# Optimization experiments

Hardware: AMD Instinct MI355X
Metric: run time of the kernel (lower is better)

## Reference

```python
import jax, jax.numpy as jnp
import numpy as np

N, F, B, H = 4096, 64, 16, 8  # nodes, feat dim, graphs, GAT heads


def _graph():
    # symmetric random graph (avg deg ~8), plus exact 2-hop and 3-hop edge lists
    # (this reproduces torch_sparse.spspmm with coalesced=True on the boolean structure)
    rng = np.random.default_rng(0)
    s = rng.integers(0, N, 8192)
    d = rng.integers(0, N, 8192)
    m = s != d
    s, d = s[m], d[m]
    rows = np.concatenate([s, d]).astype(np.int64)
    cols = np.concatenate([d, s]).astype(np.int64)
    key = np.unique(rows * N + cols)
    rows, cols = key // N, key % N
    A = np.zeros((N, N), np.float32)
    A[rows, cols] = 1.0
    A2 = (A @ A) > 0
    A3 = (A2.astype(np.float32) @ A) > 0
    np.fill_diagonal(A2, False)  # GATConv/GCNConv remove then re-add self-loops
    np.fill_diagonal(A3, False)
    e1 = np.stack([rows, cols]).astype(np.int64)
    e2 = np.stack(np.nonzero(A2)).astype(np.int64)
    e3 = np.stack(np.nonzero(A3)).astype(np.int64)
    return e1, e2, e3


def _sl(ei, n):
    loops = jnp.arange(n, dtype=ei.dtype)
    return jnp.concatenate([ei, jnp.stack([loops, loops])], axis=1)


def _seg_softmax(logits, seg, n):
    m = jax.ops.segment_max(logits, seg, num_segments=n)
    e = jnp.exp(logits - m[seg])
    s = jax.ops.segment_sum(e, seg, num_segments=n)
    return e / s[seg]


def _gat(x, ei, W, a_src, a_dst, b, heads):
    # PyG GATConv: per-head linear, edge attention logits, softmax over incoming edges
    n = x.shape[0]
    d = a_src.shape[1]
    h = (x @ W).reshape(n, heads, d)  # [N,H,D]
    src, dst = ei[0], ei[1]
    al = jnp.einsum('nhd,hd->nh', h, a_src)
    ar = jnp.einsum('nhd,hd->nh', h, a_dst)
    logit = jax.nn.leaky_relu(al[src] + ar[dst], 0.2)  # [E,H]
    alpha = _seg_softmax(logit, dst, n)
    out = jax.ops.segment_sum(alpha[:, :, None] * h[src], dst, num_segments=n)
    return out.reshape(n, heads * d) + b


def _gcn(x, ei, W, b):
    n = x.shape[0]
    src, dst = ei[0], ei[1]
    h = x @ W
    deg = jax.ops.segment_sum(jnp.ones(src.shape, x.dtype), dst, num_segments=n)
    dinv = jnp.where(deg > 0, deg ** -0.5, 0.0)
    norm = dinv[src] * dinv[dst]
    return jax.ops.segment_sum(norm[:, None] * h[src], dst, num_segments=n) + b


def setup_inputs():
    key = jax.random.key(0)
    ks = iter(jax.random.split(key, 40))
    e1, e2, e3 = _graph()
    p = lambda *shape: jax.random.normal(next(ks), shape, jnp.float32) * 0.1
    return dict(
        x=jax.random.normal(next(ks), (N, F), jnp.float32),
        edge_index=jnp.asarray(e1), edge_index2=jnp.asarray(e2), edge_index3=jnp.asarray(e3),
        batch=jnp.asarray(np.repeat(np.arange(B), N // B)),
        g1_W=p(F, H * F), g1_as=p(H, F), g1_ad=p(H, F), g1_b=p(H * F),
        g2_W=p(H * F, F), g2_as=p(1, F), g2_ad=p(1, F), g2_b=p(F),
        gfc_W=p(F, F), gfc_b=p(F), gfc1_W=p(F, 128), gfc1_b=p(128),
        gout_W=p(128, F), gout_b=p(F),
        c2_W=p(F, 2 * F), c2_b=p(2 * F), c3_W=p(2 * F, 4 * F), c3_b=p(4 * F),
        A_W=p(4 * F, F), A_b=p(F), B_W=p(2 * F, F), B_b=p(F),
        Wih=p(F, 3 * F), Whh=p(F, 3 * F), bih=p(3 * F), bhh=p(3 * F),
        f1_W=p(F, 128), f1_b=p(128), f2_W=p(128, 120), f2_b=p(120),
    )


def reference(x, edge_index, edge_index2, edge_index3, batch,
              g1_W, g1_as, g1_ad, g1_b, g2_W, g2_as, g2_ad, g2_b,
              gfc_W, gfc_b, gfc1_W, gfc1_b, gout_W, gout_b,
              c2_W, c2_b, c3_W, c3_b, A_W, A_b, B_W, B_b,
              Wih, Whh, bih, bhh, f1_W, f1_b, f2_W, f2_b):
    n = x.shape[0]
    e1, e2, e3 = _sl(edge_index, n), _sl(edge_index2, n), _sl(edge_index3, n)

    def gat_block(xin, ei):  # inner GAT module (eval mode: dropouts are identity)
        h = jax.nn.elu(_gat(xin, ei, g1_W, g1_as, g1_ad, g1_b, H))
        h = jax.nn.relu(_gat(h, ei, g2_W, g2_as, g2_ad, g2_b, 1))
        h = jax.nn.relu(h @ gfc_W + gfc_b)
        h = jax.nn.relu(h @ gfc1_W + gfc1_b)
        return h @ gout_W + gout_b

    h1 = jax.nn.relu(gat_block(x, e1))
    h2 = jax.nn.relu(_gcn(h1, e1, c2_W, c2_b))
    h3 = jax.nn.relu(_gcn(h2, e1, c3_W, c3_b))            # [N,4F]
    h4 = jax.nn.relu(gat_block(x, e2))
    h5 = jax.nn.relu(_gcn(h4, e2, c2_W, c2_b))            # [N,2F]
    h6 = jax.nn.relu(gat_block(x, e3))                     # [N,F]

    # GateUpdate
    b_ = h5 @ B_W + B_b
    a_ = h3 @ A_W + A_b
    z = jax.nn.sigmoid(a_ + b_)
    hg = z * b_ + (1 - z) * a_
    # GRUCell(h6, hg)
    gi = h6 @ Wih + bih
    gh = hg @ Whh + bhh
    r = jax.nn.sigmoid(gi[:, :F] + gh[:, :F])
    zz = jax.nn.sigmoid(gi[:, F:2 * F] + gh[:, F:2 * F])
    nn_ = jnp.tanh(gi[:, 2 * F:] + r * gh[:, 2 * F:])
    cc = (1 - zz) * nn_ + zz * hg

    g = jax.ops.segment_max(cc, batch, num_segments=B)    # global_max_pool -> [B,F]
    g = jax.nn.relu(g @ f1_W + f1_b)
    return g @ f2_W + f2_b                                 # [B,120]
```

## Files before the change

kernel.cpp:

```cpp
#include <hip/hip_runtime.h>
#include <math.h>

#define NN 4096
#define NG 16
#define WB() __builtin_amdgcn_wave_barrier()

__global__ void rowptr3_kernel(const int* __restrict__ ea, int Ea,
                               const int* __restrict__ eb, int Eb,
                               const int* __restrict__ ec, int Ec,
                               int* __restrict__ rpa, int* __restrict__ rpb, int* __restrict__ rpc){
    int t = blockIdx.x * blockDim.x + threadIdx.x;
    int set = t / (NN + 1), i = t % (NN + 1);
    if (set >= 3) return;
    const int* e0 = set == 0 ? ea : set == 1 ? eb : ec;
    int E        = set == 0 ? Ea : set == 1 ? Eb : Ec;
    int* rp      = set == 0 ? rpa : set == 1 ? rpb : rpc;
    if (i == NN){ rp[NN] = E; return; }
    int lo = 0, hi = E;
    while (lo < hi){ int mid = (lo + hi) >> 1; if (e0[mid] < i) lo = mid + 1; else hi = mid; }
    rp[i] = lo;
}

__global__ void dinv2_kernel(const int* __restrict__ rp1, const int* __restrict__ rp2,
                             float* __restrict__ dinv1, float* __restrict__ dinv2){
    int t = blockIdx.x * blockDim.x + threadIdx.x;
    int set = t >> 12, i = t & (NN - 1);
    if (set >= 2) return;
    const int* rp = set ? rp2 : rp1;
    float deg = (float)(rp[i+1] - rp[i] + 1);
    (set ? dinv2 : dinv1)[i] = 1.0f / sqrtf(deg);
}

__global__ __launch_bounds__(256)
void gemm_kernel(const float* __restrict__ A, const float* __restrict__ W,
                 const float* __restrict__ bias, float* __restrict__ C,
                 int K, int Nc, int act){
    __shared__ float As[64][17];
    __shared__ float Bs[16][64];
    const int tid = threadIdx.x;
    const int tx = tid & 15, ty = tid >> 4;
    const int row0 = blockIdx.y * 64, col0 = blockIdx.x * 64;
    float acc[4][4] = {};
    for (int k0 = 0; k0 < K; k0 += 16){
        {   int idx = tid * 4; int r = idx >> 4, kk = idx & 15;
            float4 av = *reinterpret_cast<const float4*>(&A[(size_t)(row0 + r) * K + k0 + kk]);
            As[r][kk+0]=av.x; As[r][kk+1]=av.y; As[r][kk+2]=av.z; As[r][kk+3]=av.w; }
        {   int idx = tid * 4; int r = idx >> 6, cc = idx & 63;
            float4 wv = *reinterpret_cast<const float4*>(&W[(size_t)(k0 + r) * Nc + col0 + cc]);
            *reinterpret_cast<float4*>(&Bs[r][cc]) = wv; }
        __syncthreads();
        #pragma unroll
        for (int kk = 0; kk < 16; ++kk){
            float a[4], b[4];
            #pragma unroll
            for (int i = 0; i < 4; ++i) a[i] = As[ty*4+i][kk];
            #pragma unroll
            for (int j = 0; j < 4; ++j) b[j] = Bs[kk][tx*4+j];
            #pragma unroll
            for (int i = 0; i < 4; ++i)
                #pragma unroll
                for (int j = 0; j < 4; ++j) acc[i][j] += a[i]*b[j];
        }
        __syncthreads();
    }
    #pragma unroll
    for (int i = 0; i < 4; ++i){
        int r = row0 + ty*4 + i;
        #pragma unroll
        for (int j = 0; j < 4; ++j){
            int c = col0 + tx*4 + j;
            float v = acc[i][j] + (bias ? bias[c] : 0.0f);
            if (act == 1) v = fmaxf(v, 0.0f);
            C[(size_t)r * Nc + c] = v;
        }
    }
}

__global__ __launch_bounds__(256)
void gemm_attn8_kernel(const float* __restrict__ A, const float* __restrict__ W,
                       float* __restrict__ C,
                       const float* __restrict__ a_src, const float* __restrict__ a_dst,
                       float* __restrict__ al, float* __restrict__ ar){
    __shared__ float As[64][17];
    __shared__ float Bs[16][64];
    __shared__ float redal[64][17];
    __shared__ float redar[64][17];
    const int tid = threadIdx.x;
    const int tx = tid & 15, ty = tid >> 4;
    const int row0 = blockIdx.y * 64, col0 = blockIdx.x * 64;
    const int K = 64, Nc = 512;
    float acc[4][4] = {};
    for (int k0 = 0; k0 < K; k0 += 16){
        {   int idx = tid * 4; int r = idx >> 4, kk = idx & 15;
            float4 av = *reinterpret_cast<const float4*>(&A[(size_t)(row0 + r) * K + k0 + kk]);
            As[r][kk+0]=av.x; As[r][kk+1]=av.y; As[r][kk+2]=av.z; As[r][kk+3]=av.w; }
        {   int idx = tid * 4; int r = idx >> 6, cc = idx & 63;
            float4 wv = *reinterpret_cast<const float4*>(&W[(size_t)(k0 + r) * Nc + col0 + cc]);
            *reinterpret_cast<float4*>(&Bs[r][cc]) = wv; }
        __syncthreads();
        #pragma unroll
        for (int kk = 0; kk < 16; ++kk){
            float a[4], b[4];
            #pragma unroll
            for (int i = 0; i < 4; ++i) a[i] = As[ty*4+i][kk];
            #pragma unroll
            for (int j = 0; j < 4; ++j) b[j] = Bs[kk][tx*4+j];
            #pragma unroll
            for (int i = 0; i < 4; ++i)
                #pragma unroll
                for (int j = 0; j < 4; ++j) acc[i][j] += a[i]*b[j];
        }
        __syncthreads();
    }
    float pal[4] = {0.f,0.f,0.f,0.f}, par[4] = {0.f,0.f,0.f,0.f};
    #pragma unroll
    for (int j = 0; j < 4; ++j){
        int c = col0 + tx*4 + j;
        float as = a_src[c], ad = a_dst[c];
        #pragma unroll
        for (int i = 0; i < 4; ++i){
            pal[i] += acc[i][j] * as;
            par[i] += acc[i][j] * ad;
        }
    }
    #pragma unroll
    for (int i = 0; i < 4; ++i){
        int r = row0 + ty*4 + i;
        #pragma unroll
        for (int j = 0; j < 4; ++j)
            C[(size_t)r * Nc + col0 + tx*4 + j] = acc[i][j];
        redal[ty*4+i][tx] = pal[i];
        redar[ty*4+i][tx] = par[i];
    }
    __syncthreads();
    if (tid < 64){
        float sa = 0.f, sr = 0.f;
        #pragma unroll
        for (int t = 0; t < 16; ++t){ sa += redal[tid][t]; sr += redar[tid][t]; }
        al[(size_t)(row0 + tid)*8 + blockIdx.x] = sa;
        ar[(size_t)(row0 + tid)*8 + blockIdx.x] = sr;
    }
}

__global__ __launch_bounds__(256)
void gemm32_kernel(const float* __restrict__ A, const float* __restrict__ W,
                   const float* __restrict__ bias, float* __restrict__ C,
                   int K, int Nc, int act){
    __shared__ float As[32][17];
    __shared__ float Bs[16][64];
    const int tid = threadIdx.x;
    const int tx = tid & 15, ty = tid >> 4;
    const int row0 = blockIdx.y * 32, col0 = blockIdx.x * 64;
    float acc[2][4] = {};
    for (int k0 = 0; k0 < K; k0 += 16){
        {   int idx = tid * 2; int r = idx >> 4, kk = idx & 15;
            float2 av = *reinterpret_cast<const float2*>(&A[(size_t)(row0 + r) * K + k0 + kk]);
            As[r][kk] = av.x; As[r][kk+1] = av.y; }
        {   int idx = tid * 4; int r = idx >> 6, cc = idx & 63;
            *reinterpret_cast<float4*>(&Bs[r][cc]) =
                *reinterpret_cast<const float4*>(&W[(size_t)(k0 + r) * Nc + col0 + cc]); }
        __syncthreads();
        #pragma unroll
        for (int kk = 0; kk < 16; ++kk){
            float a0 = As[ty*2][kk], a1 = As[ty*2+1][kk];
            float b[4];
            #pragma unroll
            for (int j = 0; j < 4; ++j) b[j] = Bs[kk][tx*4+j];
            #pragma unroll
            for (int j = 0; j < 4; ++j){ acc[0][j] += a0*b[j]; acc[1][j] += a1*b[j]; }
        }
        __syncthreads();
    }
    #pragma unroll
    for (int i = 0; i < 2; ++i){
        int r = row0 + ty*2 + i;
        #pragma unroll
        for (int j = 0; j < 4; ++j){
            int c = col0 + tx*4 + j;
            float v = acc[i][j] + (bias ? bias[c] : 0.0f);
            if (act == 1) v = fmaxf(v, 0.0f);
            C[(size_t)r * Nc + c] = v;
        }
    }
}

__global__ __launch_bounds__(256)
void gemm32_attn1_kernel(const float* __restrict__ A, const float* __restrict__ W,
                         float* __restrict__ C,
                         const float* __restrict__ a_src, const float* __restrict__ a_dst,
                         float* __restrict__ al, float* __restrict__ ar){
    __shared__ float As[32][17];
    __shared__ float Bs[16][64];
    __shared__ float redal[32][17];
    __shared__ float redar[32][17];
    const int tid = threadIdx.x;
    const int tx = tid & 15, ty = tid >> 4;
    const int row0 = blockIdx.y * 32;
    const int K = 512, Nc = 64;
    float acc[2][4] = {};
    for (int k0 = 0; k0 < K; k0 += 16){
        {   int idx = tid * 2; int r = idx >> 4, kk = idx & 15;
            float2 av = *reinterpret_cast<const float2*>(&A[(size_t)(row0 + r) * K + k0 + kk]);
            As[r][kk] = av.x; As[r][kk+1] = av.y; }
        {   int idx = tid * 4; int r = idx >> 6, cc = idx & 63;
            *reinterpret_cast<float4*>(&Bs[r][cc]) =
                *reinterpret_cast<const float4*>(&W[(size_t)(k0 + r) * Nc + cc]); }
        __syncthreads();
        #pragma unroll
        for (int kk = 0; kk < 16; ++kk){
            float a0 = As[ty*2][kk], a1 = As[ty*2+1][kk];
            float b[4];
            #pragma unroll
            for (int j = 0; j < 4; ++j) b[j] = Bs[kk][tx*4+j];
            #pragma unroll
            for (int j = 0; j < 4; ++j){ acc[0][j] += a0*b[j]; acc[1][j] += a1*b[j]; }
        }
        __syncthreads();
    }
    float pal[2] = {0.f,0.f}, par[2] = {0.f,0.f};
    #pragma unroll
    for (int j = 0; j < 4; ++j){
        int c = tx*4 + j;
        float as = a_src[c], ad = a_dst[c];
        pal[0] += acc[0][j]*as; pal[1] += acc[1][j]*as;
        par[0] += acc[0][j]*ad; par[1] += acc[1][j]*ad;
    }
    #pragma unroll
    for (int i = 0; i < 2; ++i){
        int r = row0 + ty*2 + i;
        #pragma unroll
        for (int j = 0; j < 4; ++j)
            C[(size_t)r * Nc + tx*4 + j] = acc[i][j];
        redal[ty*2+i][tx] = pal[i];
        redar[ty*2+i][tx] = par[i];
    }
    __syncthreads();
    if (tid < 32){
        float sa = 0.f, sr = 0.f;
        #pragma unroll
        for (int t = 0; t < 16; ++t){ sa += redal[tid][t]; sr += redar[tid][t]; }
        al[row0 + tid] = sa;
        ar[row0 + tid] = sr;
    }
}

__global__ __launch_bounds__(64)
void gat_agg8_p2_kernel(const float* __restrict__ hfeat,
                        const float* __restrict__ al, const float* __restrict__ ar,
                        const int* __restrict__ rpA, const int* __restrict__ rpB, const int* __restrict__ rpC,
                        const int* __restrict__ clA, const int* __restrict__ clB, const int* __restrict__ clC,
                        const float* __restrict__ bias, float* __restrict__ out){
    const int bid = blockIdx.x;
    const int g = bid >> 1, half = bid & 1;
    const int set = g >> 12, i = g & (NN - 1);
    const int lane = threadIdx.x;
    const int* rowptr = set == 0 ? rpA : set == 1 ? rpB : rpC;
    const int* cols   = set == 0 ? clA : set == 1 ? clB : clC;
    const int start = rowptr[i], end = rowptr[i+1];
    const int deg = end - start;
    const int hb = half * 4;
    const int c0 = half * 256 + 4 * lane;
    const int hr = lane >> 4;

    float4 arv = *reinterpret_cast<const float4*>(&ar[(size_t)i*8 + hb]);
    float ar_i[4] = {arv.x, arv.y, arv.z, arv.w};
    float4 alv = *reinterpret_cast<const float4*>(&al[(size_t)i*8 + hb]);
    float al_i[4] = {alv.x, alv.y, alv.z, alv.w};

    float mh[4], sh[4];
    #pragma unroll
    for (int h = 0; h < 4; ++h){ mh[h] = -1e30f; sh[h] = 0.f; }
    for (int k = start + lane; k < end; k += 64){
        int j = cols[k];
        float4 av = *reinterpret_cast<const float4*>(&al[(size_t)j*8 + hb]);
        float a4[4] = {av.x, av.y, av.z, av.w};
        #pragma unroll
        for (int h = 0; h < 4; ++h){
            float x = a4[h] + ar_i[h];
            x = x >= 0.f ? x : 0.2f * x;
            float mn = fmaxf(mh[h], x);
            sh[h] = sh[h] * __expf(mh[h] - mn) + __expf(x - mn);
            mh[h] = mn;
        }
    }
    if (lane == 0){
        #pragma unroll
        for (int h = 0; h < 4; ++h){
            float x = al_i[h] + ar_i[h];
            x = x >= 0.f ? x : 0.2f * x;
            float mn = fmaxf(mh[h], x);
            sh[h] = sh[h] * __expf(mh[h] - mn) + __expf(x - mn);
            mh[h] = mn;
        }
    }
    #pragma unroll
    for (int off = 1; off < 64; off <<= 1){
        #pragma unroll
        for (int h = 0; h < 4; ++h){
            float m2 = __shfl_xor(mh[h], off), s2 = __shfl_xor(sh[h], off);
            float mn = fmaxf(mh[h], m2);
            sh[h] = sh[h] * __expf(mh[h] - mn) + s2 * __expf(m2 - mn);
            mh[h] = mn;
        }
    }

    __shared__ int   sbuf[64];
    __shared__ float wbuf[64][5];
    float4 A0 = {0.f, 0.f, 0.f, 0.f};
    for (int k0 = 0; k0 < deg; k0 += 64){
        int cnt = min(64, deg - k0);
        if (lane < cnt){
            int j = cols[start + k0 + lane];
            sbuf[lane] = j;
            float4 av = *reinterpret_cast<const float4*>(&al[(size_t)j*8 + hb]);
            float a4[4] = {av.x, av.y, av.z, av.w};
            #pragma unroll
            for (int h = 0; h < 4; ++h){
                float x = a4[h] + ar_i[h];
                x = x >= 0.f ? x : 0.2f * x;
                wbuf[lane][h] = __expf(x - mh[h]);
            }
        }
        __syncthreads();
        int e = 0;
        for (; e + 8 <= cnt; e += 8){
            int j0 = sbuf[e],   j1 = sbuf[e+1], j2 = sbuf[e+2], j3 = sbuf[e+3];
            int j4 = sbuf[e+4], j5 = sbuf[e+5], j6 = sbuf[e+6], j7 = sbuf[e+7];
            float4 v0 = *reinterpret_cast<const float4*>(&hfeat[(size_t)j0*512 + c0]);
            float4 v1 = *reinterpret_cast<const float4*>(&hfeat[(size_t)j1*512 + c0]);
            float4 v2 = *reinterpret_cast<const float4*>(&hfeat[(size_t)j2*512 + c0]);
            float4 v3 = *reinterpret_cast<const float4*>(&hfeat[(size_t)j3*512 + c0]);
            float4 v4 = *reinterpret_cast<const float4*>(&hfeat[(size_t)j4*512 + c0]);
            float4 v5 = *reinterpret_cast<const float4*>(&hfeat[(size_t)j5*512 + c0]);
            float4 v6 = *reinterpret_cast<const float4*>(&hfeat[(size_t)j6*512 + c0]);
            float4 v7 = *reinterpret_cast<const float4*>(&hfeat[(size_t)j7*512 + c0]);
            float w0 = wbuf[e  ][hr], w1 = wbuf[e+1][hr], w2 = wbuf[e+2][hr], w3 = wbuf[e+3][hr];
            float w4 = wbuf[e+4][hr], w5 = wbuf[e+5][hr], w6 = wbuf[e+6][hr], w7 = wbuf[e+7][hr];
            A0.x += w0*v0.x; A0.y += w0*v0.y; A0.z += w0*v0.z; A0.w += w0*v0.w;
            A0.x += w1*v1.x; A0.y += w1*v1.y; A0.z += w1*v1.z; A0.w += w1*v1.w;
            A0.x += w2*v2.x; A0.y += w2*v2.y; A0.z += w2*v2.z; A0.w += w2*v2.w;
            A0.x += w3*v3.x; A0.y += w3*v3.y; A0.z += w3*v3.z; A0.w += w3*v3.w;
            A0.x += w4*v4.x; A0.y += w4*v4.y; A0.z += w4*v4.z; A0.w += w4*v4.w;
            A0.x += w5*v5.x; A0.y += w5*v5.y; A0.z += w5*v5.z; A0.w += w5*v5.w;
            A0.x += w6*v6.x; A0.y += w6*v6.y; A0.z += w6*v6.z; A0.w += w6*v6.w;
            A0.x += w7*v7.x; A0.y += w7*v7.y; A0.z += w7*v7.z; A0.w += w7*v7.w;
        }
        for (; e < cnt; ++e){
            int j = sbuf[e];
            float4 v = *reinterpret_cast<const float4*>(&hfeat[(size_t)j*512 + c0]);
            float w = wbuf[e][hr];
            A0.x += w*v.x; A0.y += w*v.y; A0.z += w*v.z; A0.w += w*v.w;
        }
        __syncthreads();
    }
    float x = al_i[hr] + ar_i[hr];
    x = x >= 0.f ? x : 0.2f * x;
    float ws = __expf(x - mh[hr]);
    float4 hv = *reinterpret_cast<const float4*>(&hfeat[(size_t)i*512 + c0]);
    A0.x += ws*hv.x; A0.y += ws*hv.y; A0.z += ws*hv.z; A0.w += ws*hv.w;
    float inv = 1.f / sh[hr];
    float4 bv = *reinterpret_cast<const float4*>(&bias[c0]);
    float4 o;
    o.x = A0.x*inv + bv.x; o.y = A0.y*inv + bv.y;
    o.z = A0.z*inv + bv.z; o.w = A0.w*inv + bv.w;
    o.x = o.x > 0.f ? o.x : __expf(o.x) - 1.f;
    o.y = o.y > 0.f ? o.y : __expf(o.y) - 1.f;
    o.z = o.z > 0.f ? o.z : __expf(o.z) - 1.f;
    o.w = o.w > 0.f ? o.w : __expf(o.w) - 1.f;
    *reinterpret_cast<float4*>(&out[(size_t)g*512 + c0]) = o;
}

template<int BLOCK, int NHEADS>
__global__ __launch_bounds__(BLOCK)
void gat_agg_kernel(const float* __restrict__ hfeat,
                    const float* __restrict__ al, const float* __restrict__ ar,
                    const int* __restrict__ rpA, const int* __restrict__ rpB, const int* __restrict__ rpC,
                    const int* __restrict__ clA, const int* __restrict__ clB, const int* __restrict__ clC,
                    const float* __restrict__ bias, float* __restrict__ out,
                    int act, int sharedfeat){
    constexpr int TD    = NHEADS * 64;
    constexpr int CHUNK = BLOCK / NHEADS;
    const int bid = blockIdx.x;
    const int set = bid >> 12, i = bid & (NN - 1);
    const int tid = threadIdx.x;
    const int* rowptr = set == 0 ? rpA : set == 1 ? rpB : rpC;
    const int* cols   = set == 0 ? clA : set == 1 ? clB : clC;
    const int base = sharedfeat ? 0 : set * NN;
    const int start = rowptr[i], end = rowptr[i+1];

    float al_i[NHEADS], ar_i[NHEADS];
    #pragma unroll
    for (int h = 0; h < NHEADS; ++h){
        al_i[h] = al[(size_t)(base + i)*NHEADS + h];
        ar_i[h] = ar[(size_t)(base + i)*NHEADS + h];
    }
    float m[NHEADS], s[NHEADS];
    #pragma unroll
    for (int h = 0; h < NHEADS; ++h){ m[h] = -1e30f; s[h] = 0.f; }
    for (int k = start + tid; k < end; k += BLOCK){
        int j = cols[k];
        #pragma unroll
        for (int h = 0; h < NHEADS; ++h){
            float x = al[(size_t)(base + j)*NHEADS + h] + ar_i[h];
            x = x >= 0.f ? x : 0.2f * x;
            float mn = fmaxf(m[h], x);
            s[h] = s[h] * __expf(m[h] - mn) + __expf(x - mn);
            m[h] = mn;
        }
    }
    if (tid == 0){
        #pragma unroll
        for (int h = 0; h < NHEADS; ++h){
            float x = al_i[h] + ar_i[h];
            x = x >= 0.f ? x : 0.2f * x;
            float mn = fmaxf(m[h], x);
            s[h] = s[h] * __expf(m[h] - mn) + __expf(x - mn);
            m[h] = mn;
        }
    }
    #pragma unroll
    for (int off = 1; off < 64; off <<= 1){
        #pragma unroll
        for (int h = 0; h < NHEADS; ++h){
            float m2 = __shfl_xor(m[h], off), s2 = __shfl_xor(s[h], off);
            float mn = fmaxf(m[h], m2);
            s[h] = s[h] * __expf(m[h] - mn) + s2 * __expf(m2 - mn);
            m[h] = mn;
        }
    }

    __shared__ int   sbuf[CHUNK];
    __shared__ float wbuf[CHUNK][NHEADS];
    const int deg = end - start;
    float p0 = 0.f, p1 = 0.f, p2 = 0.f, p3 = 0.f;
    for (int k0 = 0; k0 < deg; k0 += CHUNK){
        int cnt = min(CHUNK, deg - k0);
        if (tid < cnt) sbuf[tid] = cols[start + k0 + tid];
        __syncthreads();
        if (tid < cnt){
            float x = al[(size_t)(base + sbuf[tid])*NHEADS] + ar_i[0];
            x = x >= 0.f ? x : 0.2f * x;
            wbuf[tid][0] = __expf(x - m[0]);
        }
        __syncthreads();
        int e = 0;
        for (; e + 8 <= cnt; e += 8){
            int j0 = sbuf[e],   j1 = sbuf[e+1], j2 = sbuf[e+2], j3 = sbuf[e+3];
            int j4 = sbuf[e+4], j5 = sbuf[e+5], j6 = sbuf[e+6], j7 = sbuf[e+7];
            float v0 = hfeat[(size_t)(base + j0)*TD + tid];
            float v1 = hfeat[(size_t)(base + j1)*TD + tid];
            float v2 = hfeat[(size_t)(base + j2)*TD + tid];
            float v3 = hfeat[(size_t)(base + j3)*TD + tid];
            float v4 = hfeat[(size_t)(base + j4)*TD + tid];
            float v5 = hfeat[(size_t)(base + j5)*TD + tid];
            float v6 = hfeat[(size_t)(base + j6)*TD + tid];
            float v7 = hfeat[(size_t)(base + j7)*TD + tid];
            p0 += wbuf[e  ][0] * v0; p1 += wbuf[e+1][0] * v1;
            p2 += wbuf[e+2][0] * v2; p3 += wbuf[e+3][0] * v3;
            p0 += wbuf[e+4][0] * v4; p1 += wbuf[e+5][0] * v5;
            p2 += wbuf[e+6][0] * v6; p3 += wbuf[e+7][0] * v7;
        }
        for (; e < cnt; ++e)
            p0 += wbuf[e][0] * hfeat[(size_t)(base + sbuf[e])*TD + tid];
        __syncthreads();
    }
    float acc = (p0 + p1) + (p2 + p3);
    float x = al_i[0] + ar_i[0];
    x = x >= 0.f ? x : 0.2f * x;
    acc += __expf(x - m[0]) * hfeat[(size_t)(base + i)*TD + tid];
    float v = acc / s[0] + bias[tid];
    if (act == 1) v = fmaxf(v, 0.f);
    else          v = v > 0.f ? v : __expf(v) - 1.f;
    out[(size_t)bid*TD + tid] = v;
}

template<int DIM>
__global__ __launch_bounds__(DIM)
void gcn_agg_kernel(const float* __restrict__ h,
                    const int* __restrict__ rpA, const int* __restrict__ rpB,
                    const int* __restrict__ clA, const int* __restrict__ clB,
                    const float* __restrict__ dvA, const float* __restrict__ dvB,
                    const float* __restrict__ bias, float* __restrict__ out){
    const int bid = blockIdx.x;
    const int set = bid >> 12, i = bid & (NN - 1);
    const int* rowptr = set ? rpB : rpA;
    const int* cols   = set ? clB : clA;
    const float* dinv = set ? dvB : dvA;
    const int c = threadIdx.x;
    const int start = rowptr[i], end = rowptr[i+1];
    const float di = dinv[i];
    const size_t rbase = (size_t)(set * NN) * DIM;
    float self = di * di * h[(size_t)bid * DIM + c];
    float p0 = 0.f, p1 = 0.f, p2 = 0.f, p3 = 0.f;
    int k = start;
    for (; k + 8 <= end; k += 8){
        int j0 = cols[k],   j1 = cols[k+1], j2 = cols[k+2], j3 = cols[k+3];
        int j4 = cols[k+4], j5 = cols[k+5], j6 = cols[k+6], j7 = cols[k+7];
        float v0 = h[rbase + (size_t)j0 * DIM + c];
        float v1 = h[rbase + (size_t)j1 * DIM + c];
        float v2 = h[rbase + (size_t)j2 * DIM + c];
        float v3 = h[rbase + (size_t)j3 * DIM + c];
        float v4 = h[rbase + (size_t)j4 * DIM + c];
        float v5 = h[rbase + (size_t)j5 * DIM + c];
        float v6 = h[rbase + (size_t)j6 * DIM + c];
        float v7 = h[rbase + (size_t)j7 * DIM + c];
        p0 += dinv[j0] * v0; p1 += dinv[j1] * v1;
        p2 += dinv[j2] * v2; p3 += dinv[j3] * v3;
        p0 += dinv[j4] * v4; p1 += dinv[j5] * v5;
        p2 += dinv[j6] * v6; p3 += dinv[j7] * v7;
    }
    for (; k < end; ++k){
        int j = cols[k];
        p0 += dinv[j] * h[rbase + (size_t)j * DIM + c];
    }
    float acc = self + di * ((p0 + p1) + (p2 + p3));
    out[(size_t)bid * DIM + c] = fmaxf(acc + bias[c], 0.f);
}

__global__ __launch_bounds__(256)
void gate_gru_kernel(const float* __restrict__ h3, const float* __restrict__ h5,
                     const float* __restrict__ h6,
                     const float* __restrict__ A_W, const float* __restrict__ A_b,
                     const float* __restrict__ B_W, const float* __restrict__ B_b,
                     const float* __restrict__ Wih, const float* __restrict__ bih,
                     const float* __restrict__ Whh, const float* __restrict__ bhh,
                     float* __restrict__ cc){
    __shared__ float l3[4][256];
    __shared__ float l5[4][128];
    __shared__ float l6[4][64];
    __shared__ float lhg[4][64];
    const int lane = threadIdx.x & 63, wid = threadIdx.x >> 6;
    const int r = blockIdx.x * 4 + wid;
    for (int c = lane; c < 256; c += 64) l3[wid][c] = h3[(size_t)r*256 + c];
    for (int c = lane; c < 128; c += 64) l5[wid][c] = h5[(size_t)r*128 + c];
    l6[wid][lane] = h6[(size_t)r*64 + lane];
    WB();
    float a = A_b[lane];
    #pragma unroll 8
    for (int k = 0; k < 256; ++k) a += l3[wid][k] * A_W[k*64 + lane];
    float b = B_b[lane];
    #pragma unroll 8
    for (int k = 0; k < 128; ++k) b += l5[wid][k] * B_W[k*64 + lane];
    float z = 1.f / (1.f + expf(-(a + b)));
    float hg = z * b + (1.f - z) * a;
    lhg[wid][lane] = hg;
    WB();
    float gi0 = bih[lane], gi1 = bih[64 + lane], gi2 = bih[128 + lane];
    float gh0 = bhh[lane], gh1 = bhh[64 + lane], gh2 = bhh[128 + lane];
    #pragma unroll 4
    for (int k = 0; k < 64; ++k){
        float v6 = l6[wid][k], vh = lhg[wid][k];
        gi0 += v6 * Wih[k*192 + lane];
        gi1 += v6 * Wih[k*192 + 64 + lane];
        gi2 += v6 * Wih[k*192 + 128 + lane];
        gh0 += vh * Whh[k*192 + lane];
        gh1 += vh * Whh[k*192 + 64 + lane];
        gh2 += vh * Whh[k*192 + 128 + lane];
    }
    float rr = 1.f / (1.f + expf(-(gi0 + gh0)));
    float zz = 1.f / (1.f + expf(-(gi1 + gh1)));
    float nn = tanhf(gi2 + rr * gh2);
    cc[(size_t)r*64 + lane] = (1.f - zz) * nn + zz * hg;
}

__global__ __launch_bounds__(256)
void head_kernel(const float* __restrict__ cc,
                 const float* __restrict__ f1_W, const float* __restrict__ f1_b,
                 const float* __restrict__ f2_W, const float* __restrict__ f2_b,
                 float* __restrict__ out){
    const int b = blockIdx.x, tid = threadIdx.x;
    const int c = tid & 63, grp = tid >> 6;
    __shared__ float red4[4][64];
    __shared__ float gmax[64];
    __shared__ float fgs[128];
    const float* base = cc + (size_t)(b * (NN / NG)) * 64;
    float m = -1e30f;
    #pragma unroll 8
    for (int n = grp; n < NN / NG; n += 4) m = fmaxf(m, base[n * 64 + c]);
    red4[grp][c] = m;
    __syncthreads();
    if (tid < 64)
        gmax[tid] = fmaxf(fmaxf(red4[0][tid], red4[1][tid]),
                          fmaxf(red4[2][tid], red4[3][tid]));
    __syncthreads();
    if (tid < 128){
        float acc = 0.f;
        #pragma unroll
        for (int k = 0; k < 64; ++k) acc += gmax[k] * f1_W[k * 128 + tid];
        fgs[tid] = fmaxf(acc + f1_b[tid], 0.f);
    }
    __syncthreads();
    if (tid < 120){
        float acc = 0.f;
        #pragma unroll
        for (int k = 0; k < 128; ++k) acc += fgs[k] * f2_W[k * 120 + tid];
        out[b * 120 + tid] = acc + f2_b[tid];
    }
}

extern "C" void kernel_launch(void* const* d_in, const int* in_sizes, int n_in,
                              void* d_out, int out_size, void* d_ws, size_t ws_size,
                              hipStream_t stream){
    const float* x  = (const float*)d_in[0];
    const int* e1 = (const int*)d_in[1]; const int E1 = in_sizes[1] / 2;
    const int* e2 = (const int*)d_in[2]; const int E2 = in_sizes[2] / 2;
    const int* e3 = (const int*)d_in[3]; const int E3 = in_sizes[3] / 2;
    const float* g1_W  = (const float*)d_in[5];
    const float* g1_as = (const float*)d_in[6];
    const float* g1_ad = (const float*)d_in[7];
    const float* g1_b  = (const float*)d_in[8];
    const float* g2_W  = (const float*)d_in[9];
    const float* g2_as = (const float*)d_in[10];
    const float* g2_ad = (const float*)d_in[11];
    const float* g2_b  = (const float*)d_in[12];
    const float* gfc_W = (const float*)d_in[13];
    const float* gfc_b = (const float*)d_in[14];
    const float* gfc1_W= (const float*)d_in[15];
    const float* gfc1_b= (const float*)d_in[16];
    const float* gout_W= (const float*)d_in[17];
    const float* gout_b= (const float*)d_in[18];
    const float* c2_W  = (const float*)d_in[19];
    const float* c2_b  = (const float*)d_in[20];
    const float* c3_W  = (const float*)d_in[21];
    const float* c3_b  = (const float*)d_in[22];
    const float* A_W   = (const float*)d_in[23];
    const float* A_b   = (const float*)d_in[24];
    const float* B_W   = (const float*)d_in[25];
    const float* B_b   = (const float*)d_in[26];
    const float* Wih   = (const float*)d_in[27];
    const float* Whh   = (const float*)d_in[28];
    const float* bih   = (const float*)d_in[29];
    const float* bhh   = (const float*)d_in[30];
    const float* f1_W  = (const float*)d_in[31];
    const float* f1_b  = (const float*)d_in[32];
    const float* f2_W  = (const float*)d_in[33];
    const float* f2_b  = (const float*)d_in[34];
    float* out = (float*)d_out;

    int* ip = (int*)d_ws;
    int* rp1 = ip; int* rp2 = ip + 4100; int* rp3 = ip + 8200;
    float* fb = (float*)(ip + 12300);
    size_t o = 0;
    auto alloc = [&](size_t nf){ float* p = fb + o; o += nf; return p; };
    float* dinv1 = alloc(NN);
    float* dinv2 = alloc(NN);
    float* hbuf  = alloc((size_t)NN*512);
    float* al1   = alloc((size_t)NN*8);
    float* ar1   = alloc((size_t)NN*8);
    float* bigA  = alloc((size_t)3*NN*512);
    float* t2    = alloc((size_t)3*NN*64);
    float* al2   = alloc((size_t)3*NN);
    float* ar2   = alloc((size_t)3*NN);
    (void)ws_size; (void)n_in; (void)out_size;

    float* eluo3 = bigA;
    float* g2o   = bigA;
    float* fc1   = bigA + (size_t)786432;
    float* fc2   = bigA + (size_t)1572864;
    float* houts = hbuf;
    float* h1    = houts;
    float* h6    = houts + (size_t)2*NN*64;
    float* gcnx2 = bigA + (size_t)3145728;
    float* h25   = bigA + (size_t)4194304;
    float* h2    = h25;
    float* h5    = h25 + (size_t)NN*128;
    float* gcnx3 = bigA;
    float* h3    = bigA + (size_t)1048576;
    float* ccb   = bigA + (size_t)4456448;
    const int* cols1 = e1 + E1; const int* cols2 = e2 + E2; const int* cols3 = e3 + E3;

    rowptr3_kernel<<<(3*(NN+1)+255)/256, 256, 0, stream>>>(e1, E1, e2, E2, e3, E3, rp1, rp2, rp3);
    dinv2_kernel<<<2*NN/256, 256, 0, stream>>>(rp1, rp2, dinv1, dinv2);

    gemm_attn8_kernel<<<dim3(8, 64), 256, 0, stream>>>(x, g1_W, hbuf, g1_as, g1_ad, al1, ar1);
    gat_agg8_p2_kernel<<<6*NN, 64, 0, stream>>>(hbuf, al1, ar1,
        rp1, rp2, rp3, cols1, cols2, cols3, g1_b, eluo3);
    gemm32_attn1_kernel<<<dim3(1, 384), 256, 0, stream>>>(eluo3, g2_W, t2, g2_as, g2_ad, al2, ar2);
    gat_agg_kernel<64,1><<<3*NN, 64, 0, stream>>>(t2, al2, ar2,
        rp1, rp2, rp3, cols1, cols2, cols3, g2_b, g2o, 1, 0);
    gemm32_kernel<<<dim3(1, 384), 256, 0, stream>>>(g2o, gfc_W, gfc_b, fc1, 64, 64, 1);
    gemm_kernel<<<dim3(2, 192), 256, 0, stream>>>(fc1, gfc1_W, gfc1_b, fc2, 64, 128, 1);
    gemm32_kernel<<<dim3(1, 384), 256, 0, stream>>>(fc2, gout_W, gout_b, houts, 128, 64, 1);

    gemm_kernel<<<dim3(2, 128), 256, 0, stream>>>(houts, c2_W, nullptr, gcnx2, 64, 128, 0);
    gcn_agg_kernel<128><<<2*NN, 128, 0, stream>>>(gcnx2, rp1, rp2, cols1, cols2,
                                                  dinv1, dinv2, c2_b, h25);
    gemm_kernel<<<dim3(4, 64), 256, 0, stream>>>(h2, c3_W, nullptr, gcnx3, 128, 256, 0);
    gcn_agg_kernel<256><<<NN, 256, 0, stream>>>(gcnx3, rp1, rp1, cols1, cols1,
                                                dinv1, dinv1, c3_b, h3);

    gate_gru_kernel<<<NN/4, 256, 0, stream>>>(h3, h5, h6, A_W, A_b, B_W, B_b,
                                              Wih, bih, Whh, bhh, ccb);

    head_kernel<<<NG, 256, 0, stream>>>(ccb, f1_W, f1_b, f2_W, f2_b, out);
}
```

Before: 352.1 us.

## Replace per-node online softmax max pass with global max-based upper bound

A small reduction kernel now computes the global maximum of the source attention logit per head. Because leaky_relu is monotone, leaky_relu(max_al + ar_i) upper-bounds every incoming edge logit, so each node can use it as the softmax shift. This removes the separate pass over neighbours that computed an online max and sum, and the sum is now accumulated inside the main aggregation loop. The second-layer GAT aggregation is rewritten the same way as a dedicated one-head kernel. The cost is two extra single-block launches, plus a risk of exp underflow if a node's logits sit far below the global bound.

```diff
diff --git a/kernel.cpp b/kernel.cpp
--- a/kernel.cpp
+++ b/kernel.cpp
@@ -29,6 +29,31 @@
     const int* rp = set ? rp2 : rp1;
     float deg = (float)(rp[i+1] - rp[i] + 1);
     (set ? dinv2 : dinv1)[i] = 1.0f / sqrtf(deg);
+}
+
+template<int NH>
+__global__ __launch_bounds__(256)
+void max_al_kernel(const float* __restrict__ al, int n, float* __restrict__ M){
+    __shared__ float red[4 * NH];
+    float mx[NH];
+    #pragma unroll
+    for (int h = 0; h < NH; ++h) mx[h] = -1e30f;
+    for (int r = threadIdx.x; r < n; r += 256)
+        #pragma unroll
+        for (int h = 0; h < NH; ++h) mx[h] = fmaxf(mx[h], al[(size_t)r*NH + h]);
+    #pragma unroll
+    for (int h = 0; h < NH; ++h){
+        float v = mx[h];
+        #pragma unroll
+        for (int off = 1; off < 64; off <<= 1) v = fmaxf(v, __shfl_xor(v, off));
+        if ((threadIdx.x & 63) == 0) red[(threadIdx.x >> 6) * NH + h] = v;
+    }
+    __syncthreads();
+    if (threadIdx.x < NH){
+        float m = fmaxf(fmaxf(red[0*NH + threadIdx.x], red[1*NH + threadIdx.x]),
+                        fmaxf(red[2*NH + threadIdx.x], red[3*NH + threadIdx.x]));
+        M[threadIdx.x] = m;
+    }
 }
 
 __global__ __launch_bounds__(256)
@@ -247,6 +272,7 @@
 __global__ __launch_bounds__(64)
 void gat_agg8_p2_kernel(const float* __restrict__ hfeat,
                         const float* __restrict__ al, const float* __restrict__ ar,
+                        const float* __restrict__ M8,
                         const int* __restrict__ rpA, const int* __restrict__ rpB, const int* __restrict__ rpC,
                         const int* __restrict__ clA, const int* __restrict__ clB, const int* __restrict__ clC,
                         const float* __restrict__ bias, float* __restrict__ out){
@@ -266,47 +292,19 @@
     float ar_i[4] = {arv.x, arv.y, arv.z, arv.w};
     float4 alv = *reinterpret_cast<const float4*>(&al[(size_t)i*8 + hb]);
     float al_i[4] = {alv.x, alv.y, alv.z, alv.w};
-
-    float mh[4], sh[4];
-    #pragma unroll
-    for (int h = 0; h < 4; ++h){ mh[h] = -1e30f; sh[h] = 0.f; }
-    for (int k = start + lane; k < end; k += 64){
-        int j = cols[k];
-        float4 av = *reinterpret_cast<const float4*>(&al[(size_t)j*8 + hb]);
-        float a4[4] = {av.x, av.y, av.z, av.w};
-        #pragma unroll
-        for (int h = 0; h < 4; ++h){
-            float x = a4[h] + ar_i[h];
-            x = x >= 0.f ? x : 0.2f * x;
-            float mn = fmaxf(mh[h], x);
-            sh[h] = sh[h] * __expf(mh[h] - mn) + __expf(x - mn);
-            mh[h] = mn;
-        }
-    }
-    if (lane == 0){
-        #pragma unroll
-        for (int h = 0; h < 4; ++h){
-            float x = al_i[h] + ar_i[h];
-            x = x >= 0.f ? x : 0.2f * x;
-            float mn = fmaxf(mh[h], x);
-            sh[h] = sh[h] * __expf(mh[h] - mn) + __expf(x - mn);
-            mh[h] = mn;
-        }
-    }
-    #pragma unroll
-    for (int off = 1; off < 64; off <<= 1){
-        #pragma unroll
-        for (int h = 0; h < 4; ++h){
-            float m2 = __shfl_xor(mh[h], off), s2 = __shfl_xor(sh[h], off);
-            float mn = fmaxf(mh[h], m2);
-            sh[h] = sh[h] * __expf(mh[h] - mn) + s2 * __expf(m2 - mn);
-            mh[h] = mn;
-        }
+    float4 Mv = *reinterpret_cast<const float4*>(&M8[hb]);
+    float Ma[4] = {Mv.x, Mv.y, Mv.z, Mv.w};
+    float mh[4];
+    #pragma unroll
+    for (int h = 0; h < 4; ++h){
+        float t = Ma[h] + ar_i[h];
+        mh[h] = t >= 0.f ? t : 0.2f * t;
     }
 
     __shared__ int   sbuf[64];
     __shared__ float wbuf[64][5];
     float4 A0 = {0.f, 0.f, 0.f, 0.f};
+    float sacc[4] = {0.f, 0.f, 0.f, 0.f};
     for (int k0 = 0; k0 < deg; k0 += 64){
         int cnt = min(64, deg - k0);
         if (lane < cnt){
@@ -318,7 +316,9 @@
             for (int h = 0; h < 4; ++h){
                 float x = a4[h] + ar_i[h];
                 x = x >= 0.f ? x : 0.2f * x;
-                wbuf[lane][h] = __expf(x - mh[h]);
+                float w = __expf(x - mh[h]);
+                wbuf[lane][h] = w;
+                sacc[h] += w;
             }
         }
         __syncthreads();
@@ -353,12 +353,17 @@
         }
         __syncthreads();
     }
+    #pragma unroll
+    for (int off = 1; off < 64; off <<= 1){
+        #pragma unroll
+        for (int h = 0; h < 4; ++h) sacc[h] += __shfl_xor(sacc[h], off);
+    }
     float x = al_i[hr] + ar_i[hr];
     x = x >= 0.f ? x : 0.2f * x;
     float ws = __expf(x - mh[hr]);
     float4 hv = *reinterpret_cast<const float4*>(&hfeat[(size_t)i*512 + c0]);
     A0.x += ws*hv.x; A0.y += ws*hv.y; A0.z += ws*hv.z; A0.w += ws*hv.w;
-    float inv = 1.f / sh[hr];
+    float inv = 1.f / (sacc[hr] + ws);
     float4 bv = *reinterpret_cast<const float4*>(&bias[c0]);
     float4 o;
     o.x = A0.x*inv + bv.x; o.y = A0.y*inv + bv.y;
@@ -370,108 +375,73 @@
     *reinterpret_cast<float4*>(&out[(size_t)g*512 + c0]) = o;
 }
 
-template<int BLOCK, int NHEADS>
-__global__ __launch_bounds__(BLOCK)
-void gat_agg_kernel(const float* __restrict__ hfeat,
-                    const float* __restrict__ al, const float* __restrict__ ar,
-                    const int* __restrict__ rpA, const int* __restrict__ rpB, const int* __restrict__ rpC,
-                    const int* __restrict__ clA, const int* __restrict__ clB, const int* __restrict__ clC,
-                    const float* __restrict__ bias, float* __restrict__ out,
-                    int act, int sharedfeat){
-    constexpr int TD    = NHEADS * 64;
-    constexpr int CHUNK = BLOCK / NHEADS;
+__global__ __launch_bounds__(64)
+void gat_agg1_kernel(const float* __restrict__ hfeat,
+                     const float* __restrict__ al, const float* __restrict__ ar,
+                     const float* __restrict__ M1,
+                     const int* __restrict__ rpA, const int* __restrict__ rpB, const int* __restrict__ rpC,
+                     const int* __restrict__ clA, const int* __restrict__ clB, const int* __restrict__ clC,
+                     const float* __restrict__ bias, float* __restrict__ out){
     const int bid = blockIdx.x;
     const int set = bid >> 12, i = bid & (NN - 1);
     const int tid = threadIdx.x;
     const int* rowptr = set == 0 ? rpA : set == 1 ? rpB : rpC;
     const int* cols   = set == 0 ? clA : set == 1 ? clB : clC;
-    const int base = sharedfeat ? 0 : set * NN;
+    const int base = set * NN;
     const int start = rowptr[i], end = rowptr[i+1];
-
-    float al_i[NHEADS], ar_i[NHEADS];
-    #pragma unroll
-    for (int h = 0; h < NHEADS; ++h){
-        al_i[h] = al[(size_t)(base + i)*NHEADS + h];
-        ar_i[h] = ar[(size_t)(base + i)*NHEADS + h];
-    }
-    float m[NHEADS], s[NHEADS];
-    #pragma unroll
-    for (int h = 0; h < NHEADS; ++h){ m[h] = -1e30f; s[h] = 0.f; }
-    for (int k = start + tid; k < end; k += BLOCK){
-        int j = cols[k];
-        #pragma unroll
-        for (int h = 0; h < NHEADS; ++h){
-            float x = al[(size_t)(base + j)*NHEADS + h] + ar_i[h];
+    const int deg = end - start;
+
+    const float al_i = al[(size_t)base + i];
+    const float ar_i = ar[(size_t)base + i];
+    float mt = M1[0] + ar_i;
+    const float m = mt >= 0.f ? mt : 0.2f * mt;
+
+    __shared__ int   sbuf[64];
+    __shared__ float wbv[64];
+    float p0 = 0.f, p1 = 0.f, p2 = 0.f, p3 = 0.f;
+    float sacc = 0.f;
+    for (int k0 = 0; k0 < deg; k0 += 64){
+        int cnt = min(64, deg - k0);
+        if (tid < cnt){
+            int j = cols[start + k0 + tid];
+            sbuf[tid] = j;
+            float x = al[(size_t)base + j] + ar_i;
             x = x >= 0.f ? x : 0.2f * x;
-            float mn = fmaxf(m[h], x);
-            s[h] = s[h] * __expf(m[h] - mn) + __expf(x - mn);
-            m[h] = mn;
-        }
-    }
-    if (tid == 0){
-        #pragma unroll
-        for (int h = 0; h < NHEADS; ++h){
-            float x = al_i[h] + ar_i[h];
-            x = x >= 0.f ? x : 0.2f * x;
-            float mn = fmaxf(m[h], x);
-            s[h] = s[h] * __expf(m[h] - mn) + __expf(x - mn);
-            m[h] = mn;
-        }
-    }
-    #pragma unroll
-    for (int off = 1; off < 64; off <<= 1){
-        #pragma unroll
-        for (int h = 0; h < NHEADS; ++h){
-            float m2 = __shfl_xor(m[h], off), s2 = __shfl_xor(s[h], off);
-            float mn = fmaxf(m[h], m2);
-            s[h] = s[h] * __expf(m[h] - mn) + s2 * __expf(m2 - mn);
-            m[h] = mn;
-        }
-    }
-
-    __shared__ int   sbuf[CHUNK];
-    __shared__ float wbuf[CHUNK][NHEADS];
-    const int deg = end - start;
-    float p0 = 0.f, p1 = 0.f, p2 = 0.f, p3 = 0.f;
-    for (int k0 = 0; k0 < deg; k0 += CHUNK){
-        int cnt = min(CHUNK, deg - k0);
-        if (tid < cnt) sbuf[tid] = cols[start + k0 + tid];
-        __syncthreads();
-        if (tid < cnt){
-            float x = al[(size_t)(base + sbuf[tid])*NHEADS] + ar_i[0];
-            x = x >= 0.f ? x : 0.2f * x;
-            wbuf[tid][0] = __expf(x - m[0]);
+            float w = __expf(x - m);
+            wbv[tid] = w;
+            sacc += w;
         }
         __syncthreads();
         int e = 0;
         for (; e + 8 <= cnt; e += 8){
             int j0 = sbuf[e],   j1 = sbuf[e+1], j2 = sbuf[e+2], j3 = sbuf[e+3];
             int j4 = sbuf[e+4], j5 = sbuf[e+5], j6 = sbuf[e+6], j7 = sbuf[e+7];
-            float v0 = hfeat[(size_t)(base + j0)*TD + tid];
-            float v1 = hfeat[(size_t)(base + j1)*TD + tid];
-            float v2 = hfeat[(size_t)(base + j2)*TD + tid];
-            float v3 = hfeat[(size_t)(base + j3)*TD + tid];
-            float v4 = hfeat[(size_t)(base + j4)*TD + tid];
-            float v5 = hfeat[(size_t)(base + j5)*TD + tid];
-            float v6 = hfeat[(size_t)(base + j6)*TD + tid];
-            float v7 = hfeat[(size_t)(base + j7)*TD + tid];
-            p0 += wbuf[e  ][0] * v0; p1 += wbuf[e+1][0] * v1;
-            p2 += wbuf[e+2][0] * v2; p3 += wbuf[e+3][0] * v3;
-            p0 += wbuf[e+4][0] * v4; p1 += wbuf[e+5][0] * v5;
-            p2 += wbuf[e+6][0] * v6; p3 += wbuf[e+7][0] * v7;
+            float v0 = hfeat[(size_t)(base + j0)*64 + tid];
+            float v1 = hfeat[(size_t)(base + j1)*64 + tid];
+            float v2 = hfeat[(size_t)(base + j2)*64 + tid];
+            float v3 = hfeat[(size_t)(base + j3)*64 + tid];
+            float v4 = hfeat[(size_t)(base + j4)*64 + tid];
+            float v5 = hfeat[(size_t)(base + j5)*64 + tid];
+            float v6 = hfeat[(size_t)(base + j6)*64 + tid];
+            float v7 = hfeat[(size_t)(base + j7)*64 + tid];
+            p0 += wbv[e  ] * v0; p1 += wbv[e+1] * v1;
+            p2 += wbv[e+2] * v2; p3 += wbv[e+3] * v3;
+            p0 += wbv[e+4] * v4; p1 += wbv[e+5] * v5;
+            p2 += wbv[e+6] * v6; p3 += wbv[e+7] * v7;
         }
         for (; e < cnt; ++e)
-            p0 += wbuf[e][0] * hfeat[(size_t)(base + sbuf[e])*TD + tid];
-        __syncthreads();
-    }
+            p0 += wbv[e] * hfeat[(size_t)(base + sbuf[e])*64 + tid];
+        __syncthreads();
+    }
+    #pragma unroll
+    for (int off = 1; off < 64; off <<= 1) sacc += __shfl_xor(sacc, off);
     float acc = (p0 + p1) + (p2 + p3);
-    float x = al_i[0] + ar_i[0];
+    float x = al_i + ar_i;
     x = x >= 0.f ? x : 0.2f * x;
-    acc += __expf(x - m[0]) * hfeat[(size_t)(base + i)*TD + tid];
-    float v = acc / s[0] + bias[tid];
-    if (act == 1) v = fmaxf(v, 0.f);
-    else          v = v > 0.f ? v : __expf(v) - 1.f;
-    out[(size_t)bid*TD + tid] = v;
+    float ws = __expf(x - m);
+    acc += ws * hfeat[(size_t)(base + i)*64 + tid];
+    float v = acc / (sacc + ws) + bias[tid];
+    out[(size_t)bid*64 + tid] = fmaxf(v, 0.f);
 }
 
 template<int DIM>
@@ -644,6 +614,8 @@
     auto alloc = [&](size_t nf){ float* p = fb + o; o += nf; return p; };
     float* dinv1 = alloc(NN);
     float* dinv2 = alloc(NN);
+    float* M8buf = alloc(8);
+    float* M1buf = alloc(8);
     float* hbuf  = alloc((size_t)NN*512);
     float* al1   = alloc((size_t)NN*8);
     float* ar1   = alloc((size_t)NN*8);
@@ -673,11 +645,13 @@
     dinv2_kernel<<<2*NN/256, 256, 0, stream>>>(rp1, rp2, dinv1, dinv2);
 
     gemm_attn8_kernel<<<dim3(8, 64), 256, 0, stream>>>(x, g1_W, hbuf, g1_as, g1_ad, al1, ar1);
-    gat_agg8_p2_kernel<<<6*NN, 64, 0, stream>>>(hbuf, al1, ar1,
+    max_al_kernel<8><<<1, 256, 0, stream>>>(al1, NN, M8buf);
+    gat_agg8_p2_kernel<<<6*NN, 64, 0, stream>>>(hbuf, al1, ar1, M8buf,
         rp1, rp2, rp3, cols1, cols2, cols3, g1_b, eluo3);
     gemm32_attn1_kernel<<<dim3(1, 384), 256, 0, stream>>>(eluo3, g2_W, t2, g2_as, g2_ad, al2, ar2);
-    gat_agg_kernel<64,1><<<3*NN, 64, 0, stream>>>(t2, al2, ar2,
-        rp1, rp2, rp3, cols1, cols2, cols3, g2_b, g2o, 1, 0);
+    max_al_kernel<1><<<1, 256, 0, stream>>>(al2, 3*NN, M1buf);
+    gat_agg1_kernel<<<3*NN, 64, 0, stream>>>(t2, al2, ar2, M1buf,
+        rp1, rp2, rp3, cols1, cols2, cols3, g2_b, g2o);
     gemm32_kernel<<<dim3(1, 384), 256, 0, stream>>>(g2o, gfc_W, gfc_b, fc1, 64, 64, 1);
     gemm_kernel<<<dim3(2, 192), 256, 0, stream>>>(fc1, gfc1_W, gfc1_b, fc2, 64, 128, 1);
     gemm32_kernel<<<dim3(1, 384), 256, 0, stream>>>(fc2, gout_W, gout_b, houts, 128, 64, 1);
```

After: 358.5 us. No clear change (+1.8%).
